# Performance work log

Hardware: AMD Instinct MI355X
Metric: run time of the kernel (lower is better)

## Reference

```python
import jax, jax.numpy as jnp
import numpy as np

B, N, D, R = 4, 192, 128, 32


def _sh_l1(r):
    # e3nn l=1 real SH with 'integral' normalization: sqrt(3/4pi) * r_hat
    rh = r / (jnp.linalg.norm(r, axis=-1, keepdims=True) + 1e-12)
    return np.sqrt(3.0 / (4.0 * np.pi)).astype(np.float32) * rh


def _sh_l2(r):
    # l=2 real SH of unit vector, integral normalization, standard m=-2..2 order
    rh = r / (jnp.linalg.norm(r, axis=-1, keepdims=True) + 1e-12)
    x, y, z = rh[..., 0], rh[..., 1], rh[..., 2]
    c = np.float32(0.5 / np.sqrt(np.pi))
    s15 = np.float32(np.sqrt(15.0))
    s5h = np.float32(0.5 * np.sqrt(5.0))
    return c * jnp.stack([s15 * x * y, s15 * y * z, s5h * (3.0 * z * z - 1.0),
                          s15 * x * z, 0.5 * s15 * (x * x - y * y)], axis=-1)


def _radial(x, W1, b1, W2, b2):
    return jax.nn.silu(x @ W1 + b1) @ W2 + b2


def _forward(node_s, node_v, node_t, rbf, r_hat, mask,
             Ws1, bs1, Ws2, bs2, Wd1, bd1, Wd2, bd2,
             Wv1, bv1, Wv2, bv2, Wt1, bt1, Wt2, bt2,
             ln_g, ln_b, Wo, bo, v_scale, t_scale):
    m = mask[..., None]                      # (B,N,N,1)
    Y1 = _sh_l1(r_hat)                       # (B,N,N,3)
    Y2 = _sh_l2(r_hat)                       # (B,N,N,5)
    # scalar messages: h_j[b,i,j,d] = node_s[b,j,d]*mask; w0 also masked (mask applied twice, as in source)
    w0 = _radial(rbf, Ws1, bs1, Ws2, bs2) * m
    msg_s = jnp.einsum('bjd,bij,bijd->bid', node_s, mask, w0)
    # vector->scalar channel: source broadcasts node_v over j via unsqueeze(2), i.e. uses node_v of center i
    dot_vY = jnp.einsum('bimd,bijm->bijd', node_v, Y1)     # (B,N,N,D)
    w110 = _radial(rbf, Wd1, bd1, Wd2, bd2) * m
    msg_s_from_v = jnp.sum(dot_vY * w110, axis=2)          # (B,N,D)
    # CG tensor product 0e x SH -> irrep with per-channel radial weight, masked twice
    m2 = (mask * mask)[..., None]
    sj = node_s[:, None, :, :]                             # (B,1,N,D) -> broadcast over i
    wv = _radial(rbf, Wv1, bv1, Wv2, bv2)
    delta_v = jnp.einsum('bijd,bijm->bimd', m2 * wv * sj, Y1)   # (B,N,3,D)
    wt = _radial(rbf, Wt1, bt1, Wt2, bt2)
    delta_t = jnp.einsum('bijd,bijm->bimd', m2 * wt * sj, Y2)   # (B,N,5,D)
    # output scalar head: LayerNorm + Linear
    x = msg_s + msg_s_from_v
    mu = jnp.mean(x, axis=-1, keepdims=True)
    var = jnp.var(x, axis=-1, keepdims=True)
    delta_s = ((x - mu) / jnp.sqrt(var + 1e-5) * ln_g + ln_b) @ Wo + bo
    return delta_s, delta_v * v_scale, delta_t * t_scale


def setup_inputs() -> dict:
    ks = jax.random.split(jax.random.key(0), 16)
    g = lambda i, sh, s=1.0: jax.random.normal(ks[i], sh, jnp.float32) * s
    z = lambda: jnp.zeros((D,), jnp.float32)
    return dict(
        node_s=g(0, (B, N, D)), node_v=g(1, (B, N, 3, D)), node_t=g(2, (B, N, 5, D)),
        rbf=jax.random.uniform(ks[3], (B, N, N, R), jnp.float32),
        r_hat=g(4, (B, N, N, 3)), mask=jnp.ones((B, N, N), jnp.float32),
        Ws1=g(5, (R, D), 0.05), bs1=z(), Ws2=g(6, (D, D), 0.05), bs2=z(),
        Wd1=g(7, (R, D), 0.05), bd1=z(), Wd2=g(8, (D, D), 0.05), bd2=z(),
        Wv1=g(9, (R, D), 0.05), bv1=z(), Wv2=g(10, (D, D), 0.05), bv2=z(),
        Wt1=g(11, (R, D), 0.05), bt1=z(), Wt2=g(12, (D, D), 0.05), bt2=z(),
        ln_g=jnp.ones((D,), jnp.float32), ln_b=z(),
        Wo=g(13, (D, D), 0.05), bo=z(),
        v_scale=jnp.ones((D,), jnp.float32), t_scale=jnp.ones((D,), jnp.float32))


def reference(node_s, node_v, node_t, rbf, r_hat, mask,
              Ws1, bs1, Ws2, bs2, Wd1, bd1, Wd2, bd2,
              Wv1, bv1, Wv2, bv2, Wt1, bt1, Wt2, bt2,
              ln_g, ln_b, Wo, bo, v_scale, t_scale):
    return _forward(node_s, node_v, node_t, rbf, r_hat, mask,
                    Ws1, bs1, Ws2, bs2, Wd1, bd1, Wd2, bd2,
                    Wv1, bv1, Wv2, bv2, Wt1, bt1, Wt2, bt2,
                    ln_g, ln_b, Wo, bo, v_scale, t_scale)
```

## Files before the change

### kernel.cpp

```cpp
#include <hip/hip_runtime.h>
#include <hip/hip_bf16.h>

#define NB 192
#define DD 128
#define RR 32
#define RBS 40
#define SMS 132

typedef __attribute__((ext_vector_type(8))) short bf16x8;
typedef __attribute__((ext_vector_type(4))) float f32x4;

template<int M> struct IC { static constexpr int value = M; };

__device__ __forceinline__ unsigned short f2bf(float x) {
  union { __hip_bfloat16 h; unsigned short u; } c;
  c.h = __float2bfloat16(x);
  return c.u;
}
__device__ __forceinline__ float bf2f(unsigned short u) {
  union { unsigned int u; float f; } c; c.u = ((unsigned int)u) << 16;
  return c.f;
}
__device__ __forceinline__ unsigned int pack2bf(float a, float b) {
  union { unsigned short u[2]; unsigned int w; } r;
  r.u[0] = f2bf(a); r.u[1] = f2bf(b); return r.w;
}

__global__ __launch_bounds__(256) void cg_prep(
    const float* __restrict__ Ws1, const float* __restrict__ Wd1,
    const float* __restrict__ Wv1, const float* __restrict__ Wt1,
    const float* __restrict__ Ws2, const float* __restrict__ Wd2,
    const float* __restrict__ Wv2, const float* __restrict__ Wt2,
    const float* __restrict__ bs1, const float* __restrict__ bd1,
    const float* __restrict__ bv1, const float* __restrict__ bt1,
    const float* __restrict__ bs2, const float* __restrict__ bd2,
    const float* __restrict__ bv2, const float* __restrict__ bt2,
    unsigned short* __restrict__ w1f, unsigned short* __restrict__ w2f,
    float* __restrict__ bcat1, float* __restrict__ bcat2)
{
  const float* W1s[4] = {Ws1, Wd1, Wv1, Wt1};
  const float* W2s[4] = {Ws2, Wd2, Wv2, Wt2};
  const float* B1s[4] = {bs1, bd1, bv1, bt1};
  const float* B2s[4] = {bs2, bd2, bv2, bt2};
  int t = blockIdx.x * 256 + threadIdx.x;
  if (t < 2048) {
    int lane = t & 63, f = t >> 6;
    int mlp = f >> 3, htl = f & 7;
    int g = lane >> 4, ln = lane & 15;
    const float* W = W1s[mlp];
    union { unsigned short u[8]; uint4 d; } p;
    #pragma unroll
    for (int e = 0; e < 8; ++e)
      p.u[e] = f2bf(W[(8*g + e) * DD + htl*16 + ln]);
    *(uint4*)&w1f[t * 8] = p.d;
  } else if (t < 10240) {
    int t2 = t - 2048;
    int lane = t2 & 63, f = t2 >> 6;
    int ct = f & 7, ks = (f >> 3) & 3, mlp = f >> 5;
    int g = lane >> 4, ln = lane & 15;
    const float* W = W2s[mlp];
    union { unsigned short u[8]; uint4 d; } p;
    #pragma unroll
    for (int e = 0; e < 8; ++e)
      p.u[e] = f2bf(W[(32*ks + 8*g + e) * DD + ct*16 + ln]);
    *(uint4*)&w2f[t2 * 8] = p.d;
  } else if (t < 10752) {
    int t3 = t - 10240;
    bcat1[t3] = B1s[t3 >> 7][t3 & 127];
  } else if (t < 11264) {
    int t3 = t - 10752;
    bcat2[t3] = B2s[t3 >> 7][t3 & 127];
  }
}

template<int JBLK>
__global__ __launch_bounds__(256, 3) void cg_main(
    const float* __restrict__ node_s, const float* __restrict__ node_v,
    const float* __restrict__ rbf, const float* __restrict__ r_hat,
    const float* __restrict__ mask,
    const unsigned short* __restrict__ w1f, const unsigned short* __restrict__ w2f,
    const float* __restrict__ bcat1, const float* __restrict__ bcat2,
    float* __restrict__ ws)
{
  constexpr int NSPLIT = NB / JBLK;
  constexpr int NT     = JBLK / 16;
  constexpr int KSL    = JBLK / 32;
  constexpr int RB_B   = JBLK * RBS * 2;
  constexpr int HU_B   = JBLK * 128 * 2;
  constexpr int SM_B   = JBLK * SMS * 2;
  constexpr int YY_B   = 12 * JBLK * 4;
  constexpr int YA_B   = 4 * KSL * 64 * 16;
  __shared__ __align__(16) char smem[RB_B + HU_B + SM_B + YY_B + YA_B];
  unsigned short* Rb  = (unsigned short*)smem;
  unsigned short* Hu  = (unsigned short*)(smem + RB_B);
  unsigned short* SMu = (unsigned short*)(smem + RB_B + HU_B);
  float*          YYf = (float*)(smem + RB_B + HU_B + SM_B);
  unsigned short* YA  = (unsigned short*)(smem + RB_B + HU_B + SM_B + YY_B);

  const int tid  = threadIdx.x;
  const int bx   = blockIdx.x;
  const int bi   = bx / NSPLIT;
  const int jq   = bx % NSPLIT;
  const int j0   = jq * JBLK;
  const int b    = bi / NB;
  const int wid  = tid >> 6;
  const int lane = tid & 63;
  const int g = lane >> 4, ln = lane & 15;

  auto haddr = [](int j, int hb) {
    return j * 128 + (((hb) ^ ((j & 7) << 4)) >> 1);
  };

  const float* nsb = node_s + (size_t)b * (NB * DD);
  const f32x4 zacc = {0.f, 0.f, 0.f, 0.f};

  {
    const float4* rrow = (const float4*)(rbf + (size_t)bi * (NB * RR) + j0 * RR);
    #pragma unroll
    for (int f = tid; f < JBLK * 8; f += 256) {
      float4 v = rrow[f];
      union { unsigned short u[4]; uint2 d; } p;
      p.u[0] = f2bf(v.x); p.u[1] = f2bf(v.y); p.u[2] = f2bf(v.z); p.u[3] = f2bf(v.w);
      *(uint2*)&Rb[(f >> 3) * RBS + (f & 7) * 4] = p.d;
    }
  }
  if (tid < JBLK) {
    int jj = j0 + tid;
    const float* rh = r_hat + ((size_t)bi * NB + jj) * 3;
    float x = rh[0], y = rh[1], z = rh[2];
    float m = mask[(size_t)bi * NB + jj];
    float inv = 1.0f / (sqrtf(x*x + y*y + z*z) + 1e-12f);
    x *= inv; y *= inv; z *= inv;
    YYf[ 0*JBLK + tid] = m * m;
    YYf[ 1*JBLK + tid] = 0.48860252f * m * x;
    YYf[ 2*JBLK + tid] = 0.48860252f * m * y;
    YYf[ 3*JBLK + tid] = 0.48860252f * m * z;
    YYf[ 4*JBLK + tid] = 0.48860252f * x;
    YYf[ 5*JBLK + tid] = 0.48860252f * y;
    YYf[ 6*JBLK + tid] = 0.48860252f * z;
    YYf[ 7*JBLK + tid] = 1.09254843f * x * y;
    YYf[ 8*JBLK + tid] = 1.09254843f * y * z;
    YYf[ 9*JBLK + tid] = 0.31539157f * (3.f * z * z - 1.f);
    YYf[10*JBLK + tid] = 1.09254843f * x * z;
    YYf[11*JBLK + tid] = 0.54627422f * (x*x - y*y);
  }
  __syncthreads();

  #pragma unroll
  for (int i = 0; i < (JBLK * DD) / 1024; ++i) {
    int e0 = (i * 256 + tid) * 4;
    int j = e0 >> 7, d0 = e0 & 127;
    float m2 = YYf[j];
    float4 v = *(const float4*)(nsb + (size_t)(j0 + j) * DD + d0);
    union { unsigned short u[4]; uint2 dq; } p;
    p.u[0] = f2bf(m2*v.x); p.u[1] = f2bf(m2*v.y);
    p.u[2] = f2bf(m2*v.z); p.u[3] = f2bf(m2*v.w);
    *(uint2*)&SMu[j * SMS + d0] = p.dq;
  }
  for (int s = tid; s < 4 * KSL * 64; s += 256) {
    int lane_l = s & 63, rest = s >> 6;
    int ksl = rest % KSL, m = rest / KSL;
    int gl = lane_l >> 4, lnl = lane_l & 15;
    int jb0 = 32*ksl + 4*gl;
    union { unsigned short u[8]; uint4 d; } P;
    bool ok = (m == 1 && lnl >= 1 && lnl <= 3) ||
              (m == 2 && lnl >= 4 && lnl <= 6) ||
              (m == 3 && lnl >= 7 && lnl <= 11);
    if (m == 0) {
      unsigned short one = (lnl == 0) ? (unsigned short)0x3F80 : (unsigned short)0;
      #pragma unroll
      for (int e = 0; e < 8; ++e) P.u[e] = one;
    } else if (ok) {
      const float* pl = YYf + lnl * JBLK;
      float4 a = *(const float4*)(pl + jb0);
      float4 c = *(const float4*)(pl + jb0 + 16);
      P.u[0]=f2bf(a.x); P.u[1]=f2bf(a.y); P.u[2]=f2bf(a.z); P.u[3]=f2bf(a.w);
      P.u[4]=f2bf(c.x); P.u[5]=f2bf(c.y); P.u[6]=f2bf(c.z); P.u[7]=f2bf(c.w);
    } else {
      #pragma unroll
      for (int e = 0; e < 8; ++e) P.u[e] = 0;
    }
    *(uint4*)&YA[s * 8] = P.d;
  }

  const int c0 = wid * 32 + ln, c1 = c0 + 16;
  f32x4 accY0 = zacc, accY1 = zacc;

  auto run = [&](auto MC) {
    constexpr int MODE = decltype(MC)::value;
    bf16x8 Bf[4][2];
    #pragma unroll
    for (int ks = 0; ks < 4; ++ks)
      #pragma unroll
      for (int t = 0; t < 2; ++t)
        Bf[ks][t] = *(const bf16x8*)&w2f[(((MODE*4 + ks)*8 + 2*wid + t) * 64 + lane) * 8];
    float b2c0 = bcat2[MODE * DD + c0], b2c1 = bcat2[MODE * DD + c1];
    #pragma unroll
    for (int q = 0; q < 2; ++q) {
      const int htl = wid * 2 + q;
      const int f   = MODE * 8 + htl;
      bf16x8 a1 = *(const bf16x8*)&w1f[(f * 64 + lane) * 8];
      float4 b1v = *(const float4*)(bcat1 + MODE * DD + htl*16 + 4*g);
      #pragma unroll
      for (int nt = 0; nt < NT; ++nt) {
        int j = nt * 16 + ln;
        bf16x8 bb = *(const bf16x8*)&Rb[j * RBS + 8 * g];
        f32x4 h4 = __builtin_amdgcn_mfma_f32_16x16x32_bf16(a1, bb, zacc, 0, 0, 0);
        union { unsigned short u[4]; uint2 d; } hp;
        float x0 = h4[0] + b1v.x; hp.u[0] = f2bf(x0 * __builtin_amdgcn_rcpf(1.f + __expf(-x0)));
        float x1 = h4[1] + b1v.y; hp.u[1] = f2bf(x1 * __builtin_amdgcn_rcpf(1.f + __expf(-x1)));
        float x2 = h4[2] + b1v.z; hp.u[2] = f2bf(x2 * __builtin_amdgcn_rcpf(1.f + __expf(-x2)));
        float x3 = h4[3] + b1v.w; hp.u[3] = f2bf(x3 * __builtin_amdgcn_rcpf(1.f + __expf(-x3)));
        *(uint2*)&Hu[haddr(j, htl*32 + 8*g)] = hp.d;
      }
    }
    __syncthreads();
    unsigned int pw[2][NT][2];
    #pragma unroll
    for (int mt = 0; mt < NT; ++mt) {
      f32x4 acc0 = zacc, acc1 = zacc;
      #pragma unroll
      for (int ks = 0; ks < 4; ++ks) {
        bf16x8 a = *(const bf16x8*)&Hu[haddr(mt*16 + ln, ks*64 + 16*g)];
        acc0 = __builtin_amdgcn_mfma_f32_16x16x32_bf16(a, Bf[ks][0], acc0, 0, 0, 0);
        acc1 = __builtin_amdgcn_mfma_f32_16x16x32_bf16(a, Bf[ks][1], acc1, 0, 0, 0);
      }
      #pragma unroll
      for (int wd = 0; wd < 2; ++wd) {
        int jl = mt*16 + 4*g + 2*wd;
        float w00 = acc0[2*wd] + b2c0, w01 = acc0[2*wd+1] + b2c0;
        float w10 = acc1[2*wd] + b2c1, w11 = acc1[2*wd+1] + b2c1;
        float p00, p01, p10, p11;
        if constexpr (MODE == 1) {
          p00 = w00; p01 = w01; p10 = w10; p11 = w11;
        } else {
          p00 = bf2f(SMu[jl*SMS + c0]) * w00;
          p01 = bf2f(SMu[(jl+1)*SMS + c0]) * w01;
          p10 = bf2f(SMu[jl*SMS + c1]) * w10;
          p11 = bf2f(SMu[(jl+1)*SMS + c1]) * w11;
        }
        pw[0][mt][wd] = pack2bf(p00, p01);
        pw[1][mt][wd] = pack2bf(p10, p11);
      }
    }
    #pragma unroll
    for (int ksl = 0; ksl < KSL; ++ksl) {
      bf16x8 ya = *(const bf16x8*)&YA[((MODE*KSL + ksl) * 64 + lane) * 8];
      union { bf16x8 v; unsigned int w[4]; } B0, B1;
      B0.w[0] = pw[0][2*ksl][0]; B0.w[1] = pw[0][2*ksl][1];
      B0.w[2] = pw[0][2*ksl+1][0]; B0.w[3] = pw[0][2*ksl+1][1];
      B1.w[0] = pw[1][2*ksl][0]; B1.w[1] = pw[1][2*ksl][1];
      B1.w[2] = pw[1][2*ksl+1][0]; B1.w[3] = pw[1][2*ksl+1][1];
      accY0 = __builtin_amdgcn_mfma_f32_16x16x32_bf16(ya, B0.v, accY0, 0, 0, 0);
      accY1 = __builtin_amdgcn_mfma_f32_16x16x32_bf16(ya, B1.v, accY1, 0, 0, 0);
    }
    __syncthreads();
  };

  run(IC<0>{});
  run(IC<1>{});
  run(IC<2>{});
  run(IC<3>{});

  if (g < 3) {
    float* slab = ws + ((size_t)bi * NSPLIT + jq) * (12 * 128);
    #pragma unroll
    for (int r = 0; r < 4; ++r) {
      slab[(4*g + r) * 128 + c0] = accY0[r];
      slab[(4*g + r) * 128 + c1] = accY1[r];
    }
  }
}

template<int NSPLIT>
__global__ __launch_bounds__(256) void cg_final(
    const float* __restrict__ ws, const float* __restrict__ node_v,
    const float* __restrict__ ln_g, const float* __restrict__ ln_b,
    const float* __restrict__ Wo, const float* __restrict__ bo,
    const float* __restrict__ v_scale, const float* __restrict__ t_scale,
    float* __restrict__ out)
{
  __shared__ float Xv[128];
  __shared__ float XN[128];
  __shared__ float PS[2][128];
  __shared__ float ST[2];
  const int bi = blockIdx.x;
  const int tid = threadIdx.x;

  if (tid < 128) {
    float acc[12];
    #pragma unroll
    for (int k = 0; k < 12; ++k) acc[k] = 0.f;
    #pragma unroll
    for (int q = 0; q < NSPLIT; ++q) {
      const float* pa = ws + ((size_t)bi * NSPLIT + q) * (12 * 128);
      #pragma unroll
      for (int k = 0; k < 12; ++k) acc[k] += pa[k*128 + tid];
    }
    const float* nvb = node_v + (size_t)bi * (3 * DD) + tid;
    float x = acc[0] + nvb[0]*acc[1] + nvb[DD]*acc[2] + nvb[2*DD]*acc[3];
    float vs = v_scale[tid], ts = t_scale[tid];
    size_t vbase = 98304 + (size_t)bi * (3 * DD) + tid;
    out[vbase]        = acc[4] * vs;
    out[vbase + DD]   = acc[5] * vs;
    out[vbase + 2*DD] = acc[6] * vs;
    size_t tbase = 393216 + (size_t)bi * (5 * DD) + tid;
    out[tbase]        = acc[7]  * ts;
    out[tbase + DD]   = acc[8]  * ts;
    out[tbase + 2*DD] = acc[9]  * ts;
    out[tbase + 3*DD] = acc[10] * ts;
    out[tbase + 4*DD] = acc[11] * ts;
    Xv[tid] = x;
  }
  __syncthreads();
  if (tid < 64) {
    float a = Xv[tid], c = Xv[tid + 64];
    float s = a + c, ss = a*a + c*c;
    #pragma unroll
    for (int off = 32; off > 0; off >>= 1) {
      s  += __shfl_down(s, off);
      ss += __shfl_down(ss, off);
    }
    if (tid == 0) {
      float mu  = s * (1.f / 128.f);
      float var = ss * (1.f / 128.f) - mu * mu;
      ST[0] = mu; ST[1] = rsqrtf(var + 1e-5f);
    }
  }
  __syncthreads();
  if (tid < 128) XN[tid] = (Xv[tid] - ST[0]) * ST[1] * ln_g[tid] + ln_b[tid];
  __syncthreads();
  {
    int dp = tid & 127, p = tid >> 7;
    float s = 0.f;
    #pragma unroll
    for (int dd = 0; dd < 64; ++dd) {
      int d = p * 64 + dd;
      s += XN[d] * Wo[d * DD + dp];
    }
    PS[p][dp] = s;
  }
  __syncthreads();
  if (tid < 128)
    out[(size_t)bi * DD + tid] = PS[0][tid] + PS[1][tid] + bo[tid];
}

extern "C" void kernel_launch(void* const* d_in, const int* in_sizes, int n_in,
                              void* d_out, int out_size, void* d_ws, size_t ws_size,
                              hipStream_t stream) {
  (void)in_sizes; (void)n_in; (void)out_size; (void)ws_size;
  const float* node_s = (const float*)d_in[0];
  const float* node_v = (const float*)d_in[1];
  const float* rbf    = (const float*)d_in[3];
  const float* r_hat  = (const float*)d_in[4];
  const float* mask   = (const float*)d_in[5];
  const float* Ws1 = (const float*)d_in[6];  const float* bs1 = (const float*)d_in[7];
  const float* Ws2 = (const float*)d_in[8];  const float* bs2 = (const float*)d_in[9];
  const float* Wd1 = (const float*)d_in[10]; const float* bd1 = (const float*)d_in[11];
  const float* Wd2 = (const float*)d_in[12]; const float* bd2 = (const float*)d_in[13];
  const float* Wv1 = (const float*)d_in[14]; const float* bv1 = (const float*)d_in[15];
  const float* Wv2 = (const float*)d_in[16]; const float* bv2 = (const float*)d_in[17];
  const float* Wt1 = (const float*)d_in[18]; const float* bt1 = (const float*)d_in[19];
  const float* Wt2 = (const float*)d_in[20]; const float* bt2 = (const float*)d_in[21];
  const float* ln_g = (const float*)d_in[22]; const float* ln_b = (const float*)d_in[23];
  const float* Wo   = (const float*)d_in[24]; const float* bo   = (const float*)d_in[25];
  const float* v_scale = (const float*)d_in[26];
  const float* t_scale = (const float*)d_in[27];
  float* outp = (float*)d_out;

  const size_t pbytes = 768ull * 3 * 1536 * 4;
  char* wsb = (char*)d_ws;
  float* partials = (float*)wsb;
  unsigned short* w1f = (unsigned short*)(wsb + pbytes);
  unsigned short* w2f = w1f + 16384;
  float* bcat1 = (float*)(w2f + 65536);
  float* bcat2 = bcat1 + 512;

  hipLaunchKernelGGL(cg_prep, dim3(44), dim3(256), 0, stream,
                     Ws1, Wd1, Wv1, Wt1, Ws2, Wd2, Wv2, Wt2,
                     bs1, bd1, bv1, bt1, bs2, bd2, bv2, bt2,
                     w1f, w2f, bcat1, bcat2);

  hipLaunchKernelGGL((cg_main<64>), dim3(768 * 3), dim3(256), 0, stream,
                     node_s, node_v, rbf, r_hat, mask,
                     w1f, w2f, bcat1, bcat2, partials);
  hipLaunchKernelGGL((cg_final<3>), dim3(768), dim3(256), 0, stream,
                     partials, node_v, ln_g, ln_b, Wo, bo, v_scale, t_scale, outp);
}
```

Before: 64.78 us.

## Halve j-block size, reduce split partials with atomics, move mask into Y table

Changes cg_main from 64-wide to 32-wide j blocks, so 6 splits per row instead of 3, with launch bounds raised to 6 blocks per CU. Partial sums now go into one slab per row with float atomicAdd, which needs a memset, in place of per-split slabs summed in cg_final. The m² mask factor moves from the node_s staging into the Y coefficient table, so node_s loads can overlap the Y setup before the barrier. The goal is more parallelism and occupancy, at the cost of atomic contention and an extra memset launch.

Result: slower. 85.76 us (+32.4%).

```diff
diff --git a/kernel.cpp b/kernel.cpp
--- a/kernel.cpp
+++ b/kernel.cpp
@@ -74,8 +74,8 @@
 }
 
 template<int JBLK>
-__global__ __launch_bounds__(256, 3) void cg_main(
-    const float* __restrict__ node_s, const float* __restrict__ node_v,
+__global__ __launch_bounds__(256, 6) void cg_main(
+    const float* __restrict__ node_s,
     const float* __restrict__ rbf, const float* __restrict__ r_hat,
     const float* __restrict__ mask,
     const unsigned short* __restrict__ w1f, const unsigned short* __restrict__ w2f,
@@ -87,15 +87,15 @@
   constexpr int KSL    = JBLK / 32;
   constexpr int RB_B   = JBLK * RBS * 2;
   constexpr int HU_B   = JBLK * 128 * 2;
-  constexpr int SM_B   = JBLK * SMS * 2;
+  constexpr int NS_B   = JBLK * SMS * 2;
   constexpr int YY_B   = 12 * JBLK * 4;
   constexpr int YA_B   = 4 * KSL * 64 * 16;
-  __shared__ __align__(16) char smem[RB_B + HU_B + SM_B + YY_B + YA_B];
+  __shared__ __align__(16) char smem[RB_B + HU_B + NS_B + YY_B + YA_B];
   unsigned short* Rb  = (unsigned short*)smem;
   unsigned short* Hu  = (unsigned short*)(smem + RB_B);
-  unsigned short* SMu = (unsigned short*)(smem + RB_B + HU_B);
-  float*          YYf = (float*)(smem + RB_B + HU_B + SM_B);
-  unsigned short* YA  = (unsigned short*)(smem + RB_B + HU_B + SM_B + YY_B);
+  unsigned short* NSu = (unsigned short*)(smem + RB_B + HU_B);
+  float*          YYf = (float*)(smem + RB_B + HU_B + NS_B);
+  unsigned short* YA  = (unsigned short*)(smem + RB_B + HU_B + NS_B + YY_B);
 
   const int tid  = threadIdx.x;
   const int bx   = blockIdx.x;
@@ -124,6 +124,16 @@
       *(uint2*)&Rb[(f >> 3) * RBS + (f & 7) * 4] = p.d;
     }
   }
+  #pragma unroll
+  for (int i = 0; i < (JBLK * DD) / 1024; ++i) {
+    int e0 = (i * 256 + tid) * 4;
+    int j = e0 >> 7, d0 = e0 & 127;
+    float4 v = *(const float4*)(nsb + (size_t)(j0 + j) * DD + d0);
+    union { unsigned short u[4]; uint2 dq; } p;
+    p.u[0] = f2bf(v.x); p.u[1] = f2bf(v.y);
+    p.u[2] = f2bf(v.z); p.u[3] = f2bf(v.w);
+    *(uint2*)&NSu[j * SMS + d0] = p.dq;
+  }
   if (tid < JBLK) {
     int jj = j0 + tid;
     const float* rh = r_hat + ((size_t)bi * NB + jj) * 3;
@@ -131,46 +141,33 @@
     float m = mask[(size_t)bi * NB + jj];
     float inv = 1.0f / (sqrtf(x*x + y*y + z*z) + 1e-12f);
     x *= inv; y *= inv; z *= inv;
-    YYf[ 0*JBLK + tid] = m * m;
+    float m2 = m * m;
+    YYf[ 0*JBLK + tid] = m2;
     YYf[ 1*JBLK + tid] = 0.48860252f * m * x;
     YYf[ 2*JBLK + tid] = 0.48860252f * m * y;
     YYf[ 3*JBLK + tid] = 0.48860252f * m * z;
-    YYf[ 4*JBLK + tid] = 0.48860252f * x;
-    YYf[ 5*JBLK + tid] = 0.48860252f * y;
-    YYf[ 6*JBLK + tid] = 0.48860252f * z;
-    YYf[ 7*JBLK + tid] = 1.09254843f * x * y;
-    YYf[ 8*JBLK + tid] = 1.09254843f * y * z;
-    YYf[ 9*JBLK + tid] = 0.31539157f * (3.f * z * z - 1.f);
-    YYf[10*JBLK + tid] = 1.09254843f * x * z;
-    YYf[11*JBLK + tid] = 0.54627422f * (x*x - y*y);
-  }
-  __syncthreads();
-
-  #pragma unroll
-  for (int i = 0; i < (JBLK * DD) / 1024; ++i) {
-    int e0 = (i * 256 + tid) * 4;
-    int j = e0 >> 7, d0 = e0 & 127;
-    float m2 = YYf[j];
-    float4 v = *(const float4*)(nsb + (size_t)(j0 + j) * DD + d0);
-    union { unsigned short u[4]; uint2 dq; } p;
-    p.u[0] = f2bf(m2*v.x); p.u[1] = f2bf(m2*v.y);
-    p.u[2] = f2bf(m2*v.z); p.u[3] = f2bf(m2*v.w);
-    *(uint2*)&SMu[j * SMS + d0] = p.dq;
-  }
+    YYf[ 4*JBLK + tid] = 0.48860252f * m2 * x;
+    YYf[ 5*JBLK + tid] = 0.48860252f * m2 * y;
+    YYf[ 6*JBLK + tid] = 0.48860252f * m2 * z;
+    YYf[ 7*JBLK + tid] = 1.09254843f * m2 * x * y;
+    YYf[ 8*JBLK + tid] = 1.09254843f * m2 * y * z;
+    YYf[ 9*JBLK + tid] = 0.31539157f * m2 * (3.f * z * z - 1.f);
+    YYf[10*JBLK + tid] = 1.09254843f * m2 * x * z;
+    YYf[11*JBLK + tid] = 0.54627422f * m2 * (x*x - y*y);
+  }
+  __syncthreads();
+
   for (int s = tid; s < 4 * KSL * 64; s += 256) {
     int lane_l = s & 63, rest = s >> 6;
     int ksl = rest % KSL, m = rest / KSL;
     int gl = lane_l >> 4, lnl = lane_l & 15;
     int jb0 = 32*ksl + 4*gl;
     union { unsigned short u[8]; uint4 d; } P;
-    bool ok = (m == 1 && lnl >= 1 && lnl <= 3) ||
+    bool ok = (m == 0 && lnl == 0) ||
+              (m == 1 && lnl >= 1 && lnl <= 3) ||
               (m == 2 && lnl >= 4 && lnl <= 6) ||
               (m == 3 && lnl >= 7 && lnl <= 11);
-    if (m == 0) {
-      unsigned short one = (lnl == 0) ? (unsigned short)0x3F80 : (unsigned short)0;
-      #pragma unroll
-      for (int e = 0; e < 8; ++e) P.u[e] = one;
-    } else if (ok) {
+    if (ok) {
       const float* pl = YYf + lnl * JBLK;
       float4 a = *(const float4*)(pl + jb0);
       float4 c = *(const float4*)(pl + jb0 + 16);
@@ -182,6 +179,7 @@
     }
     *(uint4*)&YA[s * 8] = P.d;
   }
+  __syncthreads();
 
   const int c0 = wid * 32 + ln, c1 = c0 + 16;
   f32x4 accY0 = zacc, accY1 = zacc;
@@ -234,10 +232,10 @@
         if constexpr (MODE == 1) {
           p00 = w00; p01 = w01; p10 = w10; p11 = w11;
         } else {
-          p00 = bf2f(SMu[jl*SMS + c0]) * w00;
-          p01 = bf2f(SMu[(jl+1)*SMS + c0]) * w01;
-          p10 = bf2f(SMu[jl*SMS + c1]) * w10;
-          p11 = bf2f(SMu[(jl+1)*SMS + c1]) * w11;
+          p00 = bf2f(NSu[jl*SMS + c0]) * w00;
+          p01 = bf2f(NSu[(jl+1)*SMS + c0]) * w01;
+          p10 = bf2f(NSu[jl*SMS + c1]) * w10;
+          p11 = bf2f(NSu[(jl+1)*SMS + c1]) * w11;
         }
         pw[0][mt][wd] = pack2bf(p00, p01);
         pw[1][mt][wd] = pack2bf(p10, p11);
@@ -263,16 +261,15 @@
   run(IC<3>{});
 
   if (g < 3) {
-    float* slab = ws + ((size_t)bi * NSPLIT + jq) * (12 * 128);
+    float* slab = ws + (size_t)bi * (12 * 128);
     #pragma unroll
     for (int r = 0; r < 4; ++r) {
-      slab[(4*g + r) * 128 + c0] = accY0[r];
-      slab[(4*g + r) * 128 + c1] = accY1[r];
-    }
-  }
-}
-
-template<int NSPLIT>
+      atomicAdd(&slab[(4*g + r) * 128 + c0], accY0[r]);
+      atomicAdd(&slab[(4*g + r) * 128 + c1], accY1[r]);
+    }
+  }
+}
+
 __global__ __launch_bounds__(256) void cg_final(
     const float* __restrict__ ws, const float* __restrict__ node_v,
     const float* __restrict__ ln_g, const float* __restrict__ ln_b,
@@ -289,14 +286,9 @@
 
   if (tid < 128) {
     float acc[12];
-    #pragma unroll
-    for (int k = 0; k < 12; ++k) acc[k] = 0.f;
-    #pragma unroll
-    for (int q = 0; q < NSPLIT; ++q) {
-      const float* pa = ws + ((size_t)bi * NSPLIT + q) * (12 * 128);
-      #pragma unroll
-      for (int k = 0; k < 12; ++k) acc[k] += pa[k*128 + tid];
-    }
+    const float* pa = ws + (size_t)bi * (12 * 128);
+    #pragma unroll
+    for (int k = 0; k < 12; ++k) acc[k] = pa[k*128 + tid];
     const float* nvb = node_v + (size_t)bi * (3 * DD) + tid;
     float x = acc[0] + nvb[0]*acc[1] + nvb[DD]*acc[2] + nvb[2*DD]*acc[3];
     float vs = v_scale[tid], ts = t_scale[tid];
@@ -368,7 +360,7 @@
   const float* t_scale = (const float*)d_in[27];
   float* outp = (float*)d_out;
 
-  const size_t pbytes = 768ull * 3 * 1536 * 4;
+  const size_t pbytes = 768ull * 1536 * 4;
   char* wsb = (char*)d_ws;
   float* partials = (float*)wsb;
   unsigned short* w1f = (unsigned short*)(wsb + pbytes);
@@ -376,14 +368,15 @@
   float* bcat1 = (float*)(w2f + 65536);
   float* bcat2 = bcat1 + 512;
 
+  hipMemsetAsync(partials, 0, pbytes, stream);
   hipLaunchKernelGGL(cg_prep, dim3(44), dim3(256), 0, stream,
                      Ws1, Wd1, Wv1, Wt1, Ws2, Wd2, Wv2, Wt2,
                      bs1, bd1, bv1, bt1, bs2, bd2, bv2, bt2,
                      w1f, w2f, bcat1, bcat2);
 
-  hipLaunchKernelGGL((cg_main<64>), dim3(768 * 3), dim3(256), 0, stream,
-                     node_s, node_v, rbf, r_hat, mask,
+  hipLaunchKernelGGL((cg_main<32>), dim3(768 * 6), dim3(256), 0, stream,
+                     node_s, rbf, r_hat, mask,
                      w1f, w2f, bcat1, bcat2, partials);
-  hipLaunchKernelGGL((cg_final<3>), dim3(768), dim3(256), 0, stream,
+  hipLaunchKernelGGL(cg_final, dim3(768), dim3(256), 0, stream,
                      partials, node_v, ln_g, ln_b, Wo, bo, v_scale, t_scale, outp);
 }
```
